# Performance work log

Measured on AMD Instinct MI355X. Metric: run time of the kernel, lower is better.

## Reference

```python
import jax, jax.numpy as jnp
import numpy as np

TAU = 2.0  # aggregator_temp


def setup_inputs() -> dict:
    key = jax.random.key(0)
    k1, k2 = jax.random.split(key)
    B, Na, Nv, D = 32, 512, 256, 384
    audio_feats = jax.random.normal(k1, (B, Na, D), dtype=jnp.float32)
    visual_feats = jax.random.normal(k2, (B, Nv, D), dtype=jnp.float32)
    return {"audio_feats": audio_feats, "visual_feats": visual_feats}


def reference(audio_feats, visual_feats):
    # Cross-batch token similarities: (B, B, Na, Nv)
    # token_sims[i, j, n, m] = <audio_feats[i, n], visual_feats[j, m]>
    token_sims = jnp.einsum('ind,jmd->ijnm', audio_feats, visual_feats)
    # logsumexp_pool: tau * logsumexp(sims / tau) over key-token dim (Nv),
    # then mean over query-token dim (Na) -> clip_sims (B, B)
    aggregator = TAU * jax.nn.logsumexp(token_sims / TAU, axis=-1)
    clip_sims = aggregator.mean(axis=-1)
    return clip_sims
```

## Files before the change

kernel.cpp:

```cpp
#include <hip/hip_runtime.h>

constexpr int B_  = 32;
constexpr int Na  = 512;
constexpr int Nv  = 256;
constexpr int D   = 384;

constexpr int NK2 = D / 64;

constexpr int AGROUPS = B_ * 16;
constexpr int BGROUPS = B_ * 8;
constexpr size_t GROUP_BYTES = 12 * 1024;
constexpr int SCALE_ONE = 0x7F7F7F7F;

typedef int   int4v    __attribute__((ext_vector_type(4)));
typedef int   int8v    __attribute__((ext_vector_type(8)));
typedef float floatx16 __attribute__((ext_vector_type(16)));

__device__ __forceinline__ void async_load16(const void* g, void* l) {
    __builtin_amdgcn_global_load_lds(
        (const __attribute__((address_space(1))) unsigned int*)g,
        (__attribute__((address_space(3))) unsigned int*)l,
        16, 0, 0);
}

__global__ void convert_fp8_kernel(const float* __restrict__ a, const float* __restrict__ v,
                                   unsigned char* __restrict__ a8,
                                   unsigned char* __restrict__ b8,
                                   float* __restrict__ out) {
    int gid = blockIdx.x * blockDim.x + threadIdx.x;
    if (gid < B_ * B_) out[gid] = 0.0f;

    const float* src;
    unsigned char* dst;
    int blk = blockIdx.x;
    const bool isA = blk < AGROUPS;
    if (isA) {
        src = a + (size_t)blk * 32 * D;
        dst = a8 + (size_t)blk * GROUP_BYTES;
    } else {
        int b2 = blk - AGROUPS;
        src = v + (size_t)b2 * 32 * D;
        dst = b8 + (size_t)b2 * GROUP_BYTES;
    }
    const int t = threadIdx.x;
    const int r = t >> 3, q = t & 7;

    #pragma unroll
    for (int p = 0; p < 3; ++p) {
        int k0 = p * 128 + q * 16;
        const float4* s4 = (const float4*)(src + (size_t)r * D + k0);
        float4 f0 = s4[0], f1 = s4[1], f2 = s4[2], f3 = s4[3];
        int w0 = 0, w1 = 0, w2 = 0, w3 = 0;
        w0 = __builtin_amdgcn_cvt_pk_fp8_f32(f0.x, f0.y, w0, false);
        w0 = __builtin_amdgcn_cvt_pk_fp8_f32(f0.z, f0.w, w0, true);
        w1 = __builtin_amdgcn_cvt_pk_fp8_f32(f1.x, f1.y, w1, false);
        w1 = __builtin_amdgcn_cvt_pk_fp8_f32(f1.z, f1.w, w1, true);
        w2 = __builtin_amdgcn_cvt_pk_fp8_f32(f2.x, f2.y, w2, false);
        w2 = __builtin_amdgcn_cvt_pk_fp8_f32(f2.z, f2.w, w2, true);
        w3 = __builtin_amdgcn_cvt_pk_fp8_f32(f3.x, f3.y, w3, false);
        w3 = __builtin_amdgcn_cvt_pk_fp8_f32(f3.z, f3.w, w3, true);
        int kc = k0 >> 5;
        int h2 = (k0 >> 4) & 1;
        size_t off;
        if (isA) {
            off = (size_t)kc * 1024 + h2 * 512 + r * 16;
        } else {
            int q2 = kc >> 1, u = kc & 1, l = r + 32 * h2;
            off = (size_t)q2 * 2048 + l * 32 + u * 16;
        }
        int4v o = { w0, w1, w2, w3 };
        *(int4v*)(dst + off) = o;
    }
}

__device__ __forceinline__ float expsum16(floatx16 a) {
    constexpr float INV_TAU_LN2 = 0.7213475204444817f;
    float e[16];
    #pragma unroll
    for (int i = 0; i < 16; ++i)
        e[i] = __builtin_amdgcn_exp2f(a[i] * INV_TAU_LN2);
    float t0 = (e[0] + e[1])  + (e[2] + e[3]);
    float t1 = (e[4] + e[5])  + (e[6] + e[7]);
    float t2 = (e[8] + e[9])  + (e[10] + e[11]);
    float t3 = (e[12] + e[13]) + (e[14] + e[15]);
    return (t0 + t1) + (t2 + t3);
}

__global__ __launch_bounds__(256, 2) void gemm_lse_kernel(
        const unsigned char* __restrict__ a8,
        const unsigned char* __restrict__ b8,
        float* __restrict__ out)
{
    __shared__ unsigned char ldsA[48 * 1024];
    __shared__ float ms[4][4][32];

    const int tid  = threadIdx.x;
    const int lane = tid & 63;
    const int wn   = tid >> 6;

    int b = blockIdx.x;
    const int xcd   = b & 7;      b >>= 3;
    const int bi_lo = b & 3;      b >>= 2;
    const int rb    = b & 3;      b >>= 2;
    const int bj    = b;
    const int bi    = xcd * 4 + bi_lo;

    {
        const unsigned char* gsrc = a8 + (size_t)(bi * 16 + rb * 4 + wn) * GROUP_BYTES
                                       + (size_t)lane * 16;
        unsigned char* ldst = ldsA + (size_t)wn * GROUP_BYTES;
        #pragma unroll
        for (int kc = 0; kc < 12; ++kc)
            async_load16(gsrc + (size_t)kc * 1024, ldst + kc * 1024);
    }
    __syncthreads();

    const unsigned char* pv0 = b8 + (size_t)(bj * 8 + wn * 2) * GROUP_BYTES
                                  + (size_t)lane * 32;
    const unsigned char* pv1 = pv0 + GROUP_BYTES;
    const unsigned char* la  = ldsA + (size_t)lane * 16;

    floatx16 acc[4][2];
    #pragma unroll
    for (int g = 0; g < 4; ++g)
        #pragma unroll
        for (int vg = 0; vg < 2; ++vg)
            acc[g][vg] = (floatx16)(0.0f);

    int8v Vc0 = *(const int8v*)pv0;
    int8v Vc1 = *(const int8v*)pv1;

    #pragma unroll
    for (int q2 = 0; q2 < NK2; ++q2) {
        int8v Vn0, Vn1;
        if (q2 + 1 < NK2) {
            Vn0 = *(const int8v*)(pv0 + (size_t)(q2 + 1) * 2048);
            Vn1 = *(const int8v*)(pv1 + (size_t)(q2 + 1) * 2048);
        }
        int8v A[4];
        #pragma unroll
        for (int g = 0; g < 4; ++g) {
            const unsigned char* p = la + (size_t)g * GROUP_BYTES + (size_t)q2 * 2048;
            int4v lo = *(const int4v*)p;
            int4v hi = *(const int4v*)(p + 1024);
            A[g] = __builtin_shufflevector(lo, hi, 0, 1, 2, 3, 4, 5, 6, 7);
        }
        __builtin_amdgcn_s_setprio(1);
        #pragma unroll
        for (int g = 0; g < 4; ++g) {
            acc[g][0] = __builtin_amdgcn_mfma_scale_f32_32x32x64_f8f6f4(
                Vc0, A[g], acc[g][0], 0, 0, 0, SCALE_ONE, 0, SCALE_ONE);
            acc[g][1] = __builtin_amdgcn_mfma_scale_f32_32x32x64_f8f6f4(
                Vc1, A[g], acc[g][1], 0, 0, 0, SCALE_ONE, 0, SCALE_ONE);
        }
        __builtin_amdgcn_s_setprio(0);
        if (q2 + 1 < NK2) { Vc0 = Vn0; Vc1 = Vn1; }
    }

    float s[4];
    #pragma unroll
    for (int g = 0; g < 4; ++g) {
        s[g] = expsum16(acc[g][0]) + expsum16(acc[g][1]);
        s[g] += __shfl_xor(s[g], 32);
    }
    if (lane < 32) {
        #pragma unroll
        for (int g = 0; g < 4; ++g)
            ms[wn][g][lane] = s[g];
    }
    __syncthreads();

    if (tid < 128) {
        const int g = tid >> 5, r = tid & 31;
        float e = (ms[0][g][r] + ms[1][g][r]) + (ms[2][g][r] + ms[3][g][r]);
        constexpr float TAU_LN2 = 1.3862943611198906f;
        float lse = TAU_LN2 * __builtin_amdgcn_logf(e);
        #pragma unroll
        for (int m = 1; m < 64; m <<= 1) lse += __shfl_xor(lse, m);
        if ((tid & 63) == 0)
            atomicAdd(&out[bi * 32 + bj], lse * (1.0f / Na));
    }
}

extern "C" void kernel_launch(void* const* d_in, const int* in_sizes, int n_in,
                              void* d_out, int out_size, void* d_ws, size_t ws_size,
                              hipStream_t stream) {
    const float* audio  = (const float*)d_in[0];
    const float* visual = (const float*)d_in[1];
    float* out = (float*)d_out;

    unsigned char* a8 = (unsigned char*)d_ws;
    unsigned char* b8 = a8 + (size_t)AGROUPS * GROUP_BYTES;

    convert_fp8_kernel<<<dim3(AGROUPS + BGROUPS), dim3(256), 0, stream>>>(
        audio, visual, a8, b8, out);
    gemm_lse_kernel<<<dim3(4096), dim3(256), 0, stream>>>(a8, b8, out);
}
```

Before: 126.2 us.

## Stream V operand through double-buffered LDS with async global-to-LDS loads

The V (visual) fp8 tiles now use the same kc-major layout as A and are fetched with global_load_lds into a per-wave double buffer, with explicit vmcnt waits, instead of direct global int8v register loads. Prefetch runs two k-steps ahead, overlapping V fetch with MFMA work, and the reduction scratch reuses ldsA. This raises LDS use (80KB plus) and adds manual waitcnt and sched_barrier control, which may cut occupancy from two blocks per CU and add LDS read traffic.

```diff
diff --git a/kernel.cpp b/kernel.cpp
--- a/kernel.cpp
+++ b/kernel.cpp
@@ -33,8 +33,7 @@
     const float* src;
     unsigned char* dst;
     int blk = blockIdx.x;
-    const bool isA = blk < AGROUPS;
-    if (isA) {
+    if (blk < AGROUPS) {
         src = a + (size_t)blk * 32 * D;
         dst = a8 + (size_t)blk * GROUP_BYTES;
     } else {
@@ -61,15 +60,8 @@
         w3 = __builtin_amdgcn_cvt_pk_fp8_f32(f3.z, f3.w, w3, true);
         int kc = k0 >> 5;
         int h2 = (k0 >> 4) & 1;
-        size_t off;
-        if (isA) {
-            off = (size_t)kc * 1024 + h2 * 512 + r * 16;
-        } else {
-            int q2 = kc >> 1, u = kc & 1, l = r + 32 * h2;
-            off = (size_t)q2 * 2048 + l * 32 + u * 16;
-        }
         int4v o = { w0, w1, w2, w3 };
-        *(int4v*)(dst + off) = o;
+        *(int4v*)(dst + (size_t)kc * 1024 + h2 * 512 + r * 16) = o;
     }
 }
 
@@ -92,7 +84,8 @@
         float* __restrict__ out)
 {
     __shared__ unsigned char ldsA[48 * 1024];
-    __shared__ float ms[4][4][32];
+    __shared__ unsigned char ldsV[32 * 1024];
+    float (*ms)[4][32] = (float (*)[4][32])(void*)ldsA;
 
     const int tid  = threadIdx.x;
     const int lane = tid & 63;
@@ -105,6 +98,11 @@
     const int bj    = b;
     const int bi    = xcd * 4 + bi_lo;
 
+    const unsigned char* pv0 = b8 + (size_t)(bj * 8 + wn * 2) * GROUP_BYTES
+                                  + (size_t)lane * 16;
+    const unsigned char* pv1 = pv0 + GROUP_BYTES;
+    unsigned char* myV = ldsV + wn * 8192;
+
     {
         const unsigned char* gsrc = a8 + (size_t)(bi * 16 + rb * 4 + wn) * GROUP_BYTES
                                        + (size_t)lane * 16;
@@ -113,12 +111,17 @@
         for (int kc = 0; kc < 12; ++kc)
             async_load16(gsrc + (size_t)kc * 1024, ldst + kc * 1024);
     }
+    #pragma unroll
+    for (int q2 = 0; q2 < 2; ++q2)
+        #pragma unroll
+        for (int h = 0; h < 2; ++h) {
+            async_load16(pv0 + (size_t)(2 * q2 + h) * 1024, myV + q2 * 4096 + h * 1024);
+            async_load16(pv1 + (size_t)(2 * q2 + h) * 1024, myV + q2 * 4096 + 2048 + h * 1024);
+        }
     __syncthreads();
 
-    const unsigned char* pv0 = b8 + (size_t)(bj * 8 + wn * 2) * GROUP_BYTES
-                                  + (size_t)lane * 32;
-    const unsigned char* pv1 = pv0 + GROUP_BYTES;
-    const unsigned char* la  = ldsA + (size_t)lane * 16;
+    const unsigned char* la = ldsA + (size_t)lane * 16;
+    const unsigned char* lv = myV + (size_t)lane * 16;
 
     floatx16 acc[4][2];
     #pragma unroll
@@ -127,16 +130,19 @@
         for (int vg = 0; vg < 2; ++vg)
             acc[g][vg] = (floatx16)(0.0f);
 
-    int8v Vc0 = *(const int8v*)pv0;
-    int8v Vc1 = *(const int8v*)pv1;
-
     #pragma unroll
     for (int q2 = 0; q2 < NK2; ++q2) {
-        int8v Vn0, Vn1;
-        if (q2 + 1 < NK2) {
-            Vn0 = *(const int8v*)(pv0 + (size_t)(q2 + 1) * 2048);
-            Vn1 = *(const int8v*)(pv1 + (size_t)(q2 + 1) * 2048);
-        }
+        if (q2 < NK2 - 1) { asm volatile("s_waitcnt vmcnt(4)" ::: "memory"); }
+        else              { asm volatile("s_waitcnt vmcnt(0)" ::: "memory"); }
+        __builtin_amdgcn_sched_barrier(0);
+
+        const unsigned char* vb = lv + (q2 & 1) * 4096;
+        int4v v0lo = *(const int4v*)(vb);
+        int4v v0hi = *(const int4v*)(vb + 1024);
+        int4v v1lo = *(const int4v*)(vb + 2048);
+        int4v v1hi = *(const int4v*)(vb + 3072);
+        int8v V0 = __builtin_shufflevector(v0lo, v0hi, 0, 1, 2, 3, 4, 5, 6, 7);
+        int8v V1 = __builtin_shufflevector(v1lo, v1hi, 0, 1, 2, 3, 4, 5, 6, 7);
         int8v A[4];
         #pragma unroll
         for (int g = 0; g < 4; ++g) {
@@ -145,16 +151,27 @@
             int4v hi = *(const int4v*)(p + 1024);
             A[g] = __builtin_shufflevector(lo, hi, 0, 1, 2, 3, 4, 5, 6, 7);
         }
+        asm volatile("s_waitcnt lgkmcnt(0)" ::: "memory");
+        __builtin_amdgcn_sched_barrier(0);
+        if (q2 + 2 < NK2) {
+            #pragma unroll
+            for (int h = 0; h < 2; ++h) {
+                async_load16(pv0 + (size_t)(2 * (q2 + 2) + h) * 1024,
+                             myV + (q2 & 1) * 4096 + h * 1024);
+                async_load16(pv1 + (size_t)(2 * (q2 + 2) + h) * 1024,
+                             myV + (q2 & 1) * 4096 + 2048 + h * 1024);
+            }
+        }
+        __builtin_amdgcn_sched_barrier(0);
         __builtin_amdgcn_s_setprio(1);
         #pragma unroll
         for (int g = 0; g < 4; ++g) {
             acc[g][0] = __builtin_amdgcn_mfma_scale_f32_32x32x64_f8f6f4(
-                Vc0, A[g], acc[g][0], 0, 0, 0, SCALE_ONE, 0, SCALE_ONE);
+                V0, A[g], acc[g][0], 0, 0, 0, SCALE_ONE, 0, SCALE_ONE);
             acc[g][1] = __builtin_amdgcn_mfma_scale_f32_32x32x64_f8f6f4(
-                Vc1, A[g], acc[g][1], 0, 0, 0, SCALE_ONE, 0, SCALE_ONE);
+                V1, A[g], acc[g][1], 0, 0, 0, SCALE_ONE, 0, SCALE_ONE);
         }
         __builtin_amdgcn_s_setprio(0);
-        if (q2 + 1 < NK2) { Vc0 = Vn0; Vc1 = Vn1; }
     }
 
     float s[4];
@@ -163,6 +180,7 @@
         s[g] = expsum16(acc[g][0]) + expsum16(acc[g][1]);
         s[g] += __shfl_xor(s[g], 32);
     }
+    __syncthreads();
     if (lane < 32) {
         #pragma unroll
         for (int g = 0; g < 4; ++g)
```

Measured after the change: 126.8 us. Within noise of the previous version (+0.5%).

## Double-buffer A and V operands through LDS with per-K-step async prefetch

Applied to the files above, without the earlier changes.

Replaces the up-front whole-K load of the A tile into LDS, and the direct global V register loads, with a K-sliced double-buffered LDS pipeline. Each wave issues async global-to-LDS loads for both A and V slices of the next K step while computing the current one. V now uses the same fp8 layout as A, which simplifies the conversion kernel. The aim is to overlap global latency with MFMA work and cut LDS footprint for higher occupancy, at the cost of two block barriers per K step and explicit waitcnt management.

```diff
diff --git a/kernel.cpp b/kernel.cpp
--- a/kernel.cpp
+++ b/kernel.cpp
@@ -33,8 +33,7 @@
     const float* src;
     unsigned char* dst;
     int blk = blockIdx.x;
-    const bool isA = blk < AGROUPS;
-    if (isA) {
+    if (blk < AGROUPS) {
         src = a + (size_t)blk * 32 * D;
         dst = a8 + (size_t)blk * GROUP_BYTES;
     } else {
@@ -61,15 +60,8 @@
         w3 = __builtin_amdgcn_cvt_pk_fp8_f32(f3.z, f3.w, w3, true);
         int kc = k0 >> 5;
         int h2 = (k0 >> 4) & 1;
-        size_t off;
-        if (isA) {
-            off = (size_t)kc * 1024 + h2 * 512 + r * 16;
-        } else {
-            int q2 = kc >> 1, u = kc & 1, l = r + 32 * h2;
-            off = (size_t)q2 * 2048 + l * 32 + u * 16;
-        }
         int4v o = { w0, w1, w2, w3 };
-        *(int4v*)(dst + off) = o;
+        *(int4v*)(dst + (size_t)kc * 1024 + h2 * 512 + r * 16) = o;
     }
 }
 
@@ -91,7 +83,7 @@
         const unsigned char* __restrict__ b8,
         float* __restrict__ out)
 {
-    __shared__ unsigned char ldsA[48 * 1024];
+    __shared__ unsigned char ldsOp[2][24][1024];
     __shared__ float ms[4][4][32];
 
     const int tid  = threadIdx.x;
@@ -104,21 +96,26 @@
     const int rb    = b & 3;      b >>= 2;
     const int bj    = b;
     const int bi    = xcd * 4 + bi_lo;
-
-    {
-        const unsigned char* gsrc = a8 + (size_t)(bi * 16 + rb * 4 + wn) * GROUP_BYTES
-                                       + (size_t)lane * 16;
-        unsigned char* ldst = ldsA + (size_t)wn * GROUP_BYTES;
-        #pragma unroll
-        for (int kc = 0; kc < 12; ++kc)
-            async_load16(gsrc + (size_t)kc * 1024, ldst + kc * 1024);
-    }
-    __syncthreads();
-
-    const unsigned char* pv0 = b8 + (size_t)(bj * 8 + wn * 2) * GROUP_BYTES
-                                  + (size_t)lane * 32;
-    const unsigned char* pv1 = pv0 + GROUP_BYTES;
-    const unsigned char* la  = ldsA + (size_t)lane * 16;
+    const int aBase = bi * 16 + rb * 4;
+
+    const unsigned char* pb[6];
+    unsigned char* du0[6];
+    #pragma unroll
+    for (int i = 0; i < 6; ++i) {
+        const int u = wn * 6 + i;
+        const unsigned char* base =
+            (u < 8) ? a8 + (size_t)(aBase + (u >> 1)) * GROUP_BYTES
+                    : b8 + (size_t)(bj * 8 + ((u - 8) >> 1)) * GROUP_BYTES;
+        pb[i]  = base + (size_t)(u & 1) * 1024 + (size_t)lane * 16;
+        du0[i] = &ldsOp[0][u][0];
+    }
+
+    #pragma unroll
+    for (int i = 0; i < 6; ++i)
+        async_load16(pb[i], du0[i]);
+
+    const unsigned char* la = &ldsOp[0][0][0] + (size_t)lane * 16;
+    const unsigned char* lv = la + (size_t)(8 + 4 * wn) * 1024;
 
     floatx16 acc[4][2];
     #pragma unroll
@@ -127,34 +124,52 @@
         for (int vg = 0; vg < 2; ++vg)
             acc[g][vg] = (floatx16)(0.0f);
 
-    int8v Vc0 = *(const int8v*)pv0;
-    int8v Vc1 = *(const int8v*)pv1;
-
     #pragma unroll
     for (int q2 = 0; q2 < NK2; ++q2) {
-        int8v Vn0, Vn1;
+        const size_t bo  = (size_t)(q2 & 1) * 24576;
+        const size_t nbo = bo ^ 24576;
         if (q2 + 1 < NK2) {
-            Vn0 = *(const int8v*)(pv0 + (size_t)(q2 + 1) * 2048);
-            Vn1 = *(const int8v*)(pv1 + (size_t)(q2 + 1) * 2048);
-        }
-        int8v A[4];
+            #pragma unroll
+            for (int i = 0; i < 6; ++i)
+                async_load16(pb[i] + (size_t)(q2 + 1) * 2048, du0[i] + nbo);
+            asm volatile("s_waitcnt vmcnt(6)" ::: "memory");
+        } else {
+            asm volatile("s_waitcnt vmcnt(0)" ::: "memory");
+        }
+        __builtin_amdgcn_sched_barrier(0);
+        __builtin_amdgcn_s_barrier();
+        __builtin_amdgcn_sched_barrier(0);
+
+        int8v A[4], V0, V1;
         #pragma unroll
         for (int g = 0; g < 4; ++g) {
-            const unsigned char* p = la + (size_t)g * GROUP_BYTES + (size_t)q2 * 2048;
-            int4v lo = *(const int4v*)p;
-            int4v hi = *(const int4v*)(p + 1024);
+            int4v lo = *(const int4v*)(la + bo + (size_t)g * 2048);
+            int4v hi = *(const int4v*)(la + bo + (size_t)g * 2048 + 1024);
             A[g] = __builtin_shufflevector(lo, hi, 0, 1, 2, 3, 4, 5, 6, 7);
         }
+        {
+            int4v v0lo = *(const int4v*)(lv + bo);
+            int4v v0hi = *(const int4v*)(lv + bo + 1024);
+            int4v v1lo = *(const int4v*)(lv + bo + 2048);
+            int4v v1hi = *(const int4v*)(lv + bo + 3072);
+            V0 = __builtin_shufflevector(v0lo, v0hi, 0, 1, 2, 3, 4, 5, 6, 7);
+            V1 = __builtin_shufflevector(v1lo, v1hi, 0, 1, 2, 3, 4, 5, 6, 7);
+        }
+        asm volatile("s_waitcnt lgkmcnt(0)" ::: "memory");
+        __builtin_amdgcn_sched_barrier(0);
+
         __builtin_amdgcn_s_setprio(1);
         #pragma unroll
         for (int g = 0; g < 4; ++g) {
             acc[g][0] = __builtin_amdgcn_mfma_scale_f32_32x32x64_f8f6f4(
-                Vc0, A[g], acc[g][0], 0, 0, 0, SCALE_ONE, 0, SCALE_ONE);
+                V0, A[g], acc[g][0], 0, 0, 0, SCALE_ONE, 0, SCALE_ONE);
             acc[g][1] = __builtin_amdgcn_mfma_scale_f32_32x32x64_f8f6f4(
-                Vc1, A[g], acc[g][1], 0, 0, 0, SCALE_ONE, 0, SCALE_ONE);
+                V1, A[g], acc[g][1], 0, 0, 0, SCALE_ONE, 0, SCALE_ONE);
         }
         __builtin_amdgcn_s_setprio(0);
-        if (q2 + 1 < NK2) { Vc0 = Vn0; Vc1 = Vn1; }
+        __builtin_amdgcn_sched_barrier(0);
+        __builtin_amdgcn_s_barrier();
+        __builtin_amdgcn_sched_barrier(0);
     }
 
     float s[4];
```

After: 132.7 us. 1.05x slower.
